# Kernel optimization log

Measured on AMD Instinct MI355X. Metric: run time of the kernel, lower is better.

The kernel has to match this reference:

```python
import jax, jax.numpy as jnp
import numpy as np

LOCAL_FEATURE_WEIGHT = 1.0  # hypers['local_feature_weight']
HIDDEN = 256
X_DIM = 64
N_NODES = 512
N_GLOBAL = 8
MLP_HID = [512, 256]
N_OUT = 2


def _glorot(key, shape):
    lim = np.sqrt(6.0 / (shape[0] + shape[1]))
    return jax.random.uniform(key, shape, jnp.float32, -lim, lim)


def setup_inputs() -> dict:
    key = jax.random.key(0)
    ks = jax.random.split(key, 16)
    inp = {
        'seq': jax.random.normal(ks[0], (1024, N_NODES, X_DIM), jnp.float32),
        'global_features': jax.random.normal(ks[1], (1024, N_GLOBAL), jnp.float32),
    }
    # GRU cell params (TF GRUCell layout): gate kernel [x+h, 2h], candidate kernel [x+h, h]
    D = X_DIM + HIDDEN
    inp['fw_gw'] = _glorot(ks[2], (D, 2 * HIDDEN))
    inp['fw_gb'] = jnp.ones((2 * HIDDEN,), jnp.float32)  # TF GRUCell gate bias init = 1.0
    inp['fw_cw'] = _glorot(ks[3], (D, HIDDEN))
    inp['fw_cb'] = jnp.zeros((HIDDEN,), jnp.float32)
    inp['bw_gw'] = _glorot(ks[4], (D, 2 * HIDDEN))
    inp['bw_gb'] = jnp.ones((2 * HIDDEN,), jnp.float32)
    inp['bw_cw'] = _glorot(ks[5], (D, HIDDEN))
    inp['bw_cb'] = jnp.zeros((HIDDEN,), jnp.float32)
    # output MLP: in = 4*HIDDEN + N_GLOBAL -> 512 -> 256 -> 2
    d_in = 4 * HIDDEN + N_GLOBAL
    inp['w1'] = _glorot(ks[6], (d_in, MLP_HID[0]))
    inp['b1'] = jnp.zeros((MLP_HID[0],), jnp.float32)
    inp['w2'] = _glorot(ks[7], (MLP_HID[0], MLP_HID[1]))
    inp['b2'] = jnp.zeros((MLP_HID[1],), jnp.float32)
    inp['w3'] = _glorot(ks[8], (MLP_HID[1], N_OUT))
    inp['b3'] = jnp.zeros((N_OUT,), jnp.float32)
    return inp


def _gru_final(gw, gb, cw, cb, x):
    """TF GRUCell over x [B,T,D]; returns final hidden state [B,H]."""
    H = cb.shape[0]
    B = x.shape[0]

    def step(h, xt):
        xh = jnp.concatenate([xt, h], axis=1)
        ru = jax.nn.sigmoid(xh @ gw + gb)
        r, u = ru[:, :H], ru[:, H:]
        c = jnp.tanh(jnp.concatenate([xt, r * h], axis=1) @ cw + cb)
        h_new = u * h + (1.0 - u) * c
        return h_new, None

    h0 = jnp.zeros((B, H), x.dtype)
    hT, _ = jax.lax.scan(step, h0, jnp.swapaxes(x, 0, 1))
    return hT


def reference(seq, global_features, fw_gw, fw_gb, fw_cw, fw_cb,
              bw_gw, bw_gb, bw_cw, bw_cb, w1, b1, w2, b2, w3, b3):
    half = seq.shape[1] // 2
    target = seq[:, :half, :]
    probe = seq[:, half:, :]

    # bidirectional_dynamic_rnn final states: fw over seq, bw over reversed seq
    tgt_fw = _gru_final(fw_gw, fw_gb, fw_cw, fw_cb, target)
    tgt_bw = _gru_final(bw_gw, bw_gb, bw_cw, bw_cb, target[:, ::-1, :])
    prb_fw = _gru_final(fw_gw, fw_gb, fw_cw, fw_cb, probe)
    prb_bw = _gru_final(bw_gw, bw_gb, bw_cw, bw_cb, probe[:, ::-1, :])

    h = jnp.concatenate([tgt_fw, tgt_bw, prb_fw, prb_bw], axis=1)  # [B, 4H]
    h = jnp.concatenate([LOCAL_FEATURE_WEIGHT * h, global_features], axis=1)

    h = jax.nn.relu(h @ w1 + b1)
    h = jax.nn.relu(h @ w2 + b2)
    out = h @ w3 + b3  # [B, 2]

    pred_mean = out[:, 0]
    pred_precision = jnp.abs(out[:, 1])
    return jnp.stack([pred_mean, pred_precision], axis=1)  # [B, 2]
```

## Files before the change

kernel.cpp:

```cpp
#include <hip/hip_runtime.h>
#include <hip/hip_bf16.h>
#include <hip/hip_fp16.h>

typedef __attribute__((ext_vector_type(8))) short bf16x8;
typedef __attribute__((ext_vector_type(4))) short bf16x4;
typedef __attribute__((ext_vector_type(4))) float f32x4;
typedef __attribute__((ext_vector_type(4))) int   i32x4;

static __device__ __forceinline__ unsigned short f2bf(float f) {
  unsigned u = __float_as_uint(f);
  u += 0x7fffu + ((u >> 16) & 1u);
  return (unsigned short)(u >> 16);
}
static __device__ __forceinline__ short fb(float f) {
  union { __hip_bfloat16 b; short s; } u;
  u.b = __float2bfloat16(f);
  return u.s;
}
static __device__ __forceinline__ float sigm(float x) {
  return __builtin_amdgcn_rcpf(1.0f + __expf(-x));
}
static __device__ __forceinline__ float tanh_fast(float x) {
  return 2.0f * __builtin_amdgcn_rcpf(1.0f + __expf(-2.0f * x)) - 1.0f;
}
static __device__ __forceinline__ bf16x8 pack8(float4 a, float4 b) {
  bf16x8 v;
  v[0] = fb(a.x); v[1] = fb(a.y); v[2] = fb(a.z); v[3] = fb(a.w);
  v[4] = fb(b.x); v[5] = fb(b.y); v[6] = fb(b.z); v[7] = fb(b.w);
  return v;
}
static __device__ __forceinline__ void pin8(bf16x8& v) {
  i32x4 t;
  __builtin_memcpy(&t, &v, 16);
  asm volatile("" : "+v"(t));
  __builtin_memcpy(&v, &t, 16);
}

static __device__ __forceinline__ void lds_barrier() {
  __builtin_amdgcn_sched_barrier(0);
  asm volatile("s_waitcnt lgkmcnt(0)" ::: "memory");
  __builtin_amdgcn_s_barrier();
  __builtin_amdgcn_sched_barrier(0);
}

__global__ void prep_weights(const float* __restrict__ fw_gw, const float* __restrict__ fw_cw,
                             const float* __restrict__ bw_gw, const float* __restrict__ bw_cw,
                             unsigned short* __restrict__ wT) {
  int gid = blockIdx.x * 256 + threadIdx.x;
  int kg = gid % 80;
  int n  = (gid / 80) % 768;
  int s  = gid / (80 * 768);
  if (s >= 2) return;
  const float* gw = s ? bw_gw : fw_gw;
  const float* cw = s ? bw_cw : fw_cw;
  unsigned short* dst = wT + ((size_t)s * 768 + n) * 320 + kg * 4;
  #pragma unroll
  for (int j = 0; j < 4; ++j) {
    int k = kg * 4 + j;
    float v = (n < 512) ? gw[(size_t)k * 512 + n] : cw[(size_t)k * 256 + (n - 512)];
    dst[j] = f2bf(v);
  }
}

__global__ __attribute__((amdgpu_flat_work_group_size(512, 512), amdgpu_waves_per_eu(2, 2)))
void gru_kernel(
    const float* __restrict__ seq,
    const float* __restrict__ fw_gb, const float* __restrict__ fw_cb,
    const float* __restrict__ bw_gb, const float* __restrict__ bw_cb,
    const unsigned short* __restrict__ wT,
    float* __restrict__ h_cat) {
  __shared__ unsigned short wcLDS[256 * 256];
  __shared__ char shAB[16384];
  __shared__ __align__(16) float gbL[768];

  const int tid  = threadIdx.x;
  const int w    = tid >> 6;
  const int lane = tid & 63;
  const int l15  = lane & 15;
  const int lk   = lane >> 4;
  const int ci   = blockIdx.x >> 6;
  const int rb   = blockIdx.x & 63;
  const int s    = ci & 1;
  const int tbase = (ci >> 1) * 256;

  const unsigned short* wg = wT + (size_t)s * (768 * 320);
  const unsigned short* wc = wg + (size_t)512 * 320;
  const float* gbp = s ? bw_gb : fw_gb;
  const float* cbp = s ? bw_cb : fw_cb;

  for (int i = tid; i < 8192; i += 512) {
    const int l15s = i & 15, lks = (i >> 4) & 3, kks = (i >> 6) & 7, c16 = i >> 9;
    bf16x8 v = *(const bf16x8*)(wc + (size_t)(c16 * 16 + l15s) * 320 + 64 + kks * 32 + lks * 8);
    *(bf16x8*)((char*)wcLDS + (size_t)i * 16) = v;
  }
  for (int i = tid; i < 2048; i += 512) ((int*)shAB)[i] = 0;
  for (int i = tid; i < 768; i += 512) gbL[i] = (i < 512) ? gbp[i] : cbp[i - 512];

  const int colr = w * 32;

  bf16x8 wgr[4][10];
  #pragma unroll
  for (int nt = 0; nt < 4; ++nt) {
    const int col = (nt < 2) ? (colr + nt * 16) : (256 + colr + (nt - 2) * 16);
    const unsigned short* base = wg + (size_t)(col + l15) * 320;
    #pragma unroll
    for (int kk = 0; kk < 10; ++kk) {
      const int k = (kk < 8) ? (64 + kk * 32) : ((kk - 8) * 32);
      wgr[nt][kk] = *(const bf16x8*)(base + k + lk * 8);
    }
  }
  bf16x8 wcx[2][2];
  #pragma unroll
  for (int nt = 0; nt < 2; ++nt) {
    const unsigned short* base = wc + (size_t)(colr + nt * 16 + l15) * 320;
    #pragma unroll
    for (int kt = 0; kt < 2; ++kt)
      wcx[nt][kt] = *(const bf16x8*)(base + kt * 32 + lk * 8);
  }
  #pragma unroll
  for (int nt = 0; nt < 4; ++nt)
    #pragma unroll
    for (int kk = 0; kk < 10; ++kk) pin8(wgr[nt][kk]);
  #pragma unroll
  for (int nt = 0; nt < 2; ++nt) { pin8(wcx[nt][0]); pin8(wcx[nt][1]); }

  const int rdA = lk * 256 + l15 * 16;
  int rdB[2], wrB[2];
  #pragma unroll
  for (int nt = 0; nt < 2; ++nt) {
    rdB[nt] = (w * 2 + nt) * 8192 + lk * 256 + l15 * 16;
    const int c0 = colr + nt * 16 + lk * 4;
    wrB[nt] = ((c0 >> 5) << 10) + (((c0 >> 3) & 3) << 8) + l15 * 16 + ((c0 & 7) << 1);
  }

  const float* pseq = seq + (size_t)(rb * 16 + l15) * 32768 + lk * 8
                    + (size_t)(tbase + (s ? 255 : 0)) * 64;
  const int dstep = s ? -64 : 64;

  f32x4 hreg[2];
  hreg[0] = (f32x4)(0.f); hreg[1] = (f32x4)(0.f);

  float4 q0 = *(const float4*)(pseq);
  float4 q1 = *(const float4*)(pseq + 4);
  float4 q2 = *(const float4*)(pseq + 32);
  float4 q3 = *(const float4*)(pseq + 36);

  __syncthreads();

  #pragma unroll 1
  for (int t = 0; t < 256; ++t) {
    bf16x8 xf0 = pack8(q0, q1);
    bf16x8 xf1 = pack8(q2, q3);
    if (t != 255) {
      pseq += dstep;
      q0 = *(const float4*)(pseq);
      q1 = *(const float4*)(pseq + 4);
      q2 = *(const float4*)(pseq + 32);
      q3 = *(const float4*)(pseq + 36);
    }

    f32x4 acc1[4];
    #pragma unroll
    for (int nt = 0; nt < 4; ++nt) {
      const int g0 = ((nt < 2) ? (colr + nt * 16) : (256 + colr + (nt - 2) * 16)) + lk * 4;
      acc1[nt] = *(const f32x4*)&gbL[g0];
    }
    #pragma unroll
    for (int kk = 0; kk < 8; ++kk) {
      bf16x8 hf = *(const bf16x8*)(shAB + rdA + kk * 1024);
      #pragma unroll
      for (int nt = 0; nt < 4; ++nt)
        acc1[nt] = __builtin_amdgcn_mfma_f32_16x16x32_bf16(wgr[nt][kk], hf, acc1[nt], 0, 0, 0);
    }
    #pragma unroll
    for (int nt = 0; nt < 4; ++nt)
      acc1[nt] = __builtin_amdgcn_mfma_f32_16x16x32_bf16(wgr[nt][8], xf0, acc1[nt], 0, 0, 0);
    #pragma unroll
    for (int nt = 0; nt < 4; ++nt)
      acc1[nt] = __builtin_amdgcn_mfma_f32_16x16x32_bf16(wgr[nt][9], xf1, acc1[nt], 0, 0, 0);

    #pragma unroll
    for (int nt = 0; nt < 2; ++nt) {
      bf16x4 rhw;
      #pragma unroll
      for (int i = 0; i < 4; ++i)
        rhw[i] = fb(sigm(acc1[nt][i]) * hreg[nt][i]);
      *(bf16x4*)(shAB + 8192 + wrB[nt]) = rhw;
    }
    lds_barrier();

    f32x4 acc2[2];
    #pragma unroll
    for (int nt = 0; nt < 2; ++nt)
      acc2[nt] = *(const f32x4*)&gbL[512 + colr + nt * 16 + lk * 4];
    #pragma unroll
    for (int kk = 0; kk < 8; ++kk) {
      bf16x8 rh = *(const bf16x8*)(shAB + 8192 + rdA + kk * 1024);
      #pragma unroll
      for (int nt = 0; nt < 2; ++nt) {
        bf16x8 b = *(const bf16x8*)((const char*)wcLDS + rdB[nt] + kk * 1024);
        acc2[nt] = __builtin_amdgcn_mfma_f32_16x16x32_bf16(b, rh, acc2[nt], 0, 0, 0);
      }
    }
    #pragma unroll
    for (int nt = 0; nt < 2; ++nt) {
      acc2[nt] = __builtin_amdgcn_mfma_f32_16x16x32_bf16(wcx[nt][0], xf0, acc2[nt], 0, 0, 0);
      acc2[nt] = __builtin_amdgcn_mfma_f32_16x16x32_bf16(wcx[nt][1], xf1, acc2[nt], 0, 0, 0);
    }

    const bool last = (t == 255);
    #pragma unroll
    for (int nt = 0; nt < 2; ++nt) {
      bf16x4 hw;
      float hc[4];
      #pragma unroll
      for (int i = 0; i < 4; ++i) {
        const float cv = tanh_fast(acc2[nt][i]);
        const float u  = sigm(acc1[nt + 2][i]);
        const float hn = u * hreg[nt][i] + (1.f - u) * cv;
        hreg[nt][i] = hn;
        hw[i] = fb(hn);
        hc[i] = hn;
      }
      *(bf16x4*)(shAB + wrB[nt]) = hw;
      if (last) {
        float4 o; o.x = hc[0]; o.y = hc[1]; o.z = hc[2]; o.w = hc[3];
        *(float4*)&h_cat[(size_t)(rb * 16 + l15) * 1024 + ci * 256 + colr + nt * 16 + lk * 4] = o;
      }
    }
    lds_barrier();
  }
}

__global__ __launch_bounds__(256) void mlp1(const float* __restrict__ h_cat,
                                            const float* __restrict__ gf,
                                            const float* __restrict__ w1,
                                            const float* __restrict__ b1,
                                            float* __restrict__ a1) {
  __shared__ float xs[8][1036];
  const int tid = threadIdx.x;
  const int r0 = blockIdx.x * 8;
  for (int i = tid; i < 8 * 1032; i += 256) {
    int m = i / 1032, k = i - m * 1032;
    xs[m][k] = (k < 1024) ? h_cat[(size_t)(r0 + m) * 1024 + k]
                          : gf[(size_t)(r0 + m) * 8 + (k - 1024)];
  }
  __syncthreads();
  float acc0[8], acc1v[8];
  #pragma unroll
  for (int m = 0; m < 8; ++m) { acc0[m] = 0.f; acc1v[m] = 0.f; }
  const int n = tid;
  for (int k = 0; k < 1032; k += 4) {
    float wa[4], wb[4];
    #pragma unroll
    for (int j = 0; j < 4; ++j) {
      wa[j] = w1[(size_t)(k + j) * 512 + n];
      wb[j] = w1[(size_t)(k + j) * 512 + n + 256];
    }
    #pragma unroll
    for (int m = 0; m < 8; ++m) {
      float4 xv = *(const float4*)&xs[m][k];
      acc0[m]  = fmaf(xv.w, wa[3], fmaf(xv.z, wa[2], fmaf(xv.y, wa[1], fmaf(xv.x, wa[0], acc0[m]))));
      acc1v[m] = fmaf(xv.w, wb[3], fmaf(xv.z, wb[2], fmaf(xv.y, wb[1], fmaf(xv.x, wb[0], acc1v[m]))));
    }
  }
  const float bb0 = b1[n], bb1 = b1[n + 256];
  #pragma unroll
  for (int m = 0; m < 8; ++m) {
    a1[(size_t)(r0 + m) * 512 + n]       = fmaxf(acc0[m] + bb0, 0.f);
    a1[(size_t)(r0 + m) * 512 + n + 256] = fmaxf(acc1v[m] + bb1, 0.f);
  }
}

__global__ __launch_bounds__(256) void mlp2(const float* __restrict__ a1,
                                            const float* __restrict__ w2,
                                            const float* __restrict__ b2,
                                            float* __restrict__ a2) {
  __shared__ float xs[8][516];
  const int tid = threadIdx.x;
  const int r0 = blockIdx.x * 8;
  for (int i = tid; i < 8 * 512; i += 256) {
    int m = i >> 9, k = i & 511;
    xs[m][k] = a1[(size_t)(r0 + m) * 512 + k];
  }
  __syncthreads();
  float acc[8];
  #pragma unroll
  for (int m = 0; m < 8; ++m) acc[m] = 0.f;
  for (int k = 0; k < 512; k += 4) {
    float wa[4];
    #pragma unroll
    for (int j = 0; j < 4; ++j) wa[j] = w2[(size_t)(k + j) * 256 + tid];
    #pragma unroll
    for (int m = 0; m < 8; ++m) {
      float4 xv = *(const float4*)&xs[m][k];
      acc[m] = fmaf(xv.w, wa[3], fmaf(xv.z, wa[2], fmaf(xv.y, wa[1], fmaf(xv.x, wa[0], acc[m]))));
    }
  }
  const float bb = b2[tid];
  #pragma unroll
  for (int m = 0; m < 8; ++m)
    a2[(size_t)(r0 + m) * 256 + tid] = fmaxf(acc[m] + bb, 0.f);
}

__global__ __launch_bounds__(256) void mlp3(const float* __restrict__ a2,
                                            const float* __restrict__ w3,
                                            const float* __restrict__ b3,
                                            float* __restrict__ out) {
  const int r = blockIdx.x * 256 + threadIdx.x;
  float m = 0.f, p = 0.f;
  for (int k = 0; k < 256; k += 4) {
    float4 v = *(const float4*)&a2[(size_t)r * 256 + k];
    m = fmaf(v.x, w3[2 * k],     fmaf(v.y, w3[2 * k + 2], fmaf(v.z, w3[2 * k + 4], fmaf(v.w, w3[2 * k + 6], m))));
    p = fmaf(v.x, w3[2 * k + 1], fmaf(v.y, w3[2 * k + 3], fmaf(v.z, w3[2 * k + 5], fmaf(v.w, w3[2 * k + 7], p))));
  }
  out[2 * r]     = m + b3[0];
  out[2 * r + 1] = fabsf(p + b3[1]);
}

extern "C" void kernel_launch(void* const* d_in, const int* in_sizes, int n_in,
                              void* d_out, int out_size, void* d_ws, size_t ws_size,
                              hipStream_t stream) {
  const float* seq   = (const float*)d_in[0];
  const float* gf    = (const float*)d_in[1];
  const float* fw_gw = (const float*)d_in[2];
  const float* fw_gb = (const float*)d_in[3];
  const float* fw_cw = (const float*)d_in[4];
  const float* fw_cb = (const float*)d_in[5];
  const float* bw_gw = (const float*)d_in[6];
  const float* bw_gb = (const float*)d_in[7];
  const float* bw_cw = (const float*)d_in[8];
  const float* bw_cb = (const float*)d_in[9];
  const float* w1 = (const float*)d_in[10];
  const float* b1 = (const float*)d_in[11];
  const float* w2 = (const float*)d_in[12];
  const float* b2 = (const float*)d_in[13];
  const float* w3 = (const float*)d_in[14];
  const float* b3 = (const float*)d_in[15];
  float* out = (float*)d_out;

  char* ws = (char*)d_ws;
  unsigned short* wT = (unsigned short*)(ws);
  float* h_cat = (float*)(ws + 983040);
  float* a1    = (float*)(ws + 983040 + 4194304);
  float* a2    = (float*)(ws + 983040 + 4194304 + 2097152);

  hipLaunchKernelGGL(prep_weights, dim3(480), dim3(256), 0, stream,
                     fw_gw, fw_cw, bw_gw, bw_cw, wT);
  hipLaunchKernelGGL(gru_kernel, dim3(256), dim3(512), 0, stream,
                     seq, fw_gb, fw_cb, bw_gb, bw_cb, wT, h_cat);
  hipLaunchKernelGGL(mlp1, dim3(128), dim3(256), 0, stream, h_cat, gf, w1, b1, a1);
  hipLaunchKernelGGL(mlp2, dim3(128), dim3(256), 0, stream, a1, w2, b2, a2);
  hipLaunchKernelGGL(mlp3, dim3(4), dim3(256), 0, stream, a2, w3, b3, out);
}
```

Measured before the change: 723.9 us.

## Move x-input MFMAs off the recurrent critical path and split accumulator chains

The input-projection MFMAs for the next timestep's gate accumulators are issued at the end of the current step, after the hidden-state write. The candidate's x-projection is issued before the LDS barrier rather than after the r*h matmul. The r*h matmul uses two interleaved accumulators to shorten the dependent MFMA chain, and the update-gate sigmoid is computed early. The aim is to cut serial latency per recurrent step. The cost is extra registers and a slightly different summation order.

```diff
diff --git a/kernel.cpp b/kernel.cpp
--- a/kernel.cpp
+++ b/kernel.cpp
@@ -144,90 +144,108 @@
   float4 q1 = *(const float4*)(pseq + 4);
   float4 q2 = *(const float4*)(pseq + 32);
   float4 q3 = *(const float4*)(pseq + 36);
+  bf16x8 xf0 = pack8(q0, q1);
+  bf16x8 xf1 = pack8(q2, q3);
+  pseq += dstep;
+  q0 = *(const float4*)(pseq);
+  q1 = *(const float4*)(pseq + 4);
+  q2 = *(const float4*)(pseq + 32);
+  q3 = *(const float4*)(pseq + 36);
 
   __syncthreads();
+
+  f32x4 acc1[4];
+  #pragma unroll
+  for (int nt = 0; nt < 4; ++nt) {
+    const int g0 = ((nt < 2) ? (colr + nt * 16) : (256 + colr + (nt - 2) * 16)) + lk * 4;
+    acc1[nt] = *(const f32x4*)&gbL[g0];
+    acc1[nt] = __builtin_amdgcn_mfma_f32_16x16x32_bf16(wgr[nt][8], xf0, acc1[nt], 0, 0, 0);
+    acc1[nt] = __builtin_amdgcn_mfma_f32_16x16x32_bf16(wgr[nt][9], xf1, acc1[nt], 0, 0, 0);
+  }
 
   #pragma unroll 1
   for (int t = 0; t < 256; ++t) {
-    bf16x8 xf0 = pack8(q0, q1);
-    bf16x8 xf1 = pack8(q2, q3);
-    if (t != 255) {
-      pseq += dstep;
+    #pragma unroll
+    for (int kk = 0; kk < 8; ++kk) {
+      bf16x8 hf = *(const bf16x8*)(shAB + rdA + kk * 1024);
+      #pragma unroll
+      for (int nt = 0; nt < 4; ++nt)
+        acc1[nt] = __builtin_amdgcn_mfma_f32_16x16x32_bf16(wgr[nt][kk], hf, acc1[nt], 0, 0, 0);
+    }
+
+    float ur[2][4];
+    #pragma unroll
+    for (int nt = 0; nt < 2; ++nt) {
+      bf16x4 rhw;
+      #pragma unroll
+      for (int i = 0; i < 4; ++i) {
+        rhw[i] = fb(sigm(acc1[nt][i]) * hreg[nt][i]);
+        ur[nt][i] = sigm(acc1[nt + 2][i]);
+      }
+      *(bf16x4*)(shAB + 8192 + wrB[nt]) = rhw;
+    }
+
+    f32x4 acc2[2];
+    #pragma unroll
+    for (int nt = 0; nt < 2; ++nt) {
+      acc2[nt] = *(const f32x4*)&gbL[512 + colr + nt * 16 + lk * 4];
+      acc2[nt] = __builtin_amdgcn_mfma_f32_16x16x32_bf16(wcx[nt][0], xf0, acc2[nt], 0, 0, 0);
+      acc2[nt] = __builtin_amdgcn_mfma_f32_16x16x32_bf16(wcx[nt][1], xf1, acc2[nt], 0, 0, 0);
+    }
+
+    lds_barrier();
+
+    f32x4 acc2o[2];
+    acc2o[0] = (f32x4)(0.f); acc2o[1] = (f32x4)(0.f);
+    #pragma unroll
+    for (int kk = 0; kk < 8; ++kk) {
+      bf16x8 rh = *(const bf16x8*)(shAB + 8192 + rdA + kk * 1024);
+      #pragma unroll
+      for (int nt = 0; nt < 2; ++nt) {
+        bf16x8 b = *(const bf16x8*)((const char*)wcLDS + rdB[nt] + kk * 1024);
+        if (kk & 1)
+          acc2o[nt] = __builtin_amdgcn_mfma_f32_16x16x32_bf16(b, rh, acc2o[nt], 0, 0, 0);
+        else
+          acc2[nt]  = __builtin_amdgcn_mfma_f32_16x16x32_bf16(b, rh, acc2[nt], 0, 0, 0);
+      }
+    }
+
+    const bool last = (t == 255);
+    #pragma unroll
+    for (int nt = 0; nt < 2; ++nt) {
+      f32x4 a2 = acc2[nt] + acc2o[nt];
+      bf16x4 hw;
+      #pragma unroll
+      for (int i = 0; i < 4; ++i) {
+        const float cv = tanh_fast(a2[i]);
+        const float hn = cv + ur[nt][i] * (hreg[nt][i] - cv);
+        hreg[nt][i] = hn;
+        hw[i] = fb(hn);
+      }
+      *(bf16x4*)(shAB + wrB[nt]) = hw;
+      if (last) {
+        float4 o; o.x = hreg[nt][0]; o.y = hreg[nt][1]; o.z = hreg[nt][2]; o.w = hreg[nt][3];
+        *(float4*)&h_cat[(size_t)(rb * 16 + l15) * 1024 + ci * 256 + colr + nt * 16 + lk * 4] = o;
+      }
+    }
+
+    if (t < 255) {
+      xf0 = pack8(q0, q1);
+      xf1 = pack8(q2, q3);
+      pseq = (t < 254) ? (pseq + dstep) : pseq;
       q0 = *(const float4*)(pseq);
       q1 = *(const float4*)(pseq + 4);
       q2 = *(const float4*)(pseq + 32);
       q3 = *(const float4*)(pseq + 36);
-    }
-
-    f32x4 acc1[4];
-    #pragma unroll
-    for (int nt = 0; nt < 4; ++nt) {
-      const int g0 = ((nt < 2) ? (colr + nt * 16) : (256 + colr + (nt - 2) * 16)) + lk * 4;
-      acc1[nt] = *(const f32x4*)&gbL[g0];
-    }
-    #pragma unroll
-    for (int kk = 0; kk < 8; ++kk) {
-      bf16x8 hf = *(const bf16x8*)(shAB + rdA + kk * 1024);
-      #pragma unroll
-      for (int nt = 0; nt < 4; ++nt)
-        acc1[nt] = __builtin_amdgcn_mfma_f32_16x16x32_bf16(wgr[nt][kk], hf, acc1[nt], 0, 0, 0);
-    }
-    #pragma unroll
-    for (int nt = 0; nt < 4; ++nt)
-      acc1[nt] = __builtin_amdgcn_mfma_f32_16x16x32_bf16(wgr[nt][8], xf0, acc1[nt], 0, 0, 0);
-    #pragma unroll
-    for (int nt = 0; nt < 4; ++nt)
-      acc1[nt] = __builtin_amdgcn_mfma_f32_16x16x32_bf16(wgr[nt][9], xf1, acc1[nt], 0, 0, 0);
-
-    #pragma unroll
-    for (int nt = 0; nt < 2; ++nt) {
-      bf16x4 rhw;
-      #pragma unroll
-      for (int i = 0; i < 4; ++i)
-        rhw[i] = fb(sigm(acc1[nt][i]) * hreg[nt][i]);
-      *(bf16x4*)(shAB + 8192 + wrB[nt]) = rhw;
-    }
-    lds_barrier();
-
-    f32x4 acc2[2];
-    #pragma unroll
-    for (int nt = 0; nt < 2; ++nt)
-      acc2[nt] = *(const f32x4*)&gbL[512 + colr + nt * 16 + lk * 4];
-    #pragma unroll
-    for (int kk = 0; kk < 8; ++kk) {
-      bf16x8 rh = *(const bf16x8*)(shAB + 8192 + rdA + kk * 1024);
-      #pragma unroll
-      for (int nt = 0; nt < 2; ++nt) {
-        bf16x8 b = *(const bf16x8*)((const char*)wcLDS + rdB[nt] + kk * 1024);
-        acc2[nt] = __builtin_amdgcn_mfma_f32_16x16x32_bf16(b, rh, acc2[nt], 0, 0, 0);
-      }
-    }
-    #pragma unroll
-    for (int nt = 0; nt < 2; ++nt) {
-      acc2[nt] = __builtin_amdgcn_mfma_f32_16x16x32_bf16(wcx[nt][0], xf0, acc2[nt], 0, 0, 0);
-      acc2[nt] = __builtin_amdgcn_mfma_f32_16x16x32_bf16(wcx[nt][1], xf1, acc2[nt], 0, 0, 0);
-    }
-
-    const bool last = (t == 255);
-    #pragma unroll
-    for (int nt = 0; nt < 2; ++nt) {
-      bf16x4 hw;
-      float hc[4];
-      #pragma unroll
-      for (int i = 0; i < 4; ++i) {
-        const float cv = tanh_fast(acc2[nt][i]);
-        const float u  = sigm(acc1[nt + 2][i]);
-        const float hn = u * hreg[nt][i] + (1.f - u) * cv;
-        hreg[nt][i] = hn;
-        hw[i] = fb(hn);
-        hc[i] = hn;
-      }
-      *(bf16x4*)(shAB + wrB[nt]) = hw;
-      if (last) {
-        float4 o; o.x = hc[0]; o.y = hc[1]; o.z = hc[2]; o.w = hc[3];
-        *(float4*)&h_cat[(size_t)(rb * 16 + l15) * 1024 + ci * 256 + colr + nt * 16 + lk * 4] = o;
-      }
-    }
+      #pragma unroll
+      for (int nt = 0; nt < 4; ++nt) {
+        const int g0 = ((nt < 2) ? (colr + nt * 16) : (256 + colr + (nt - 2) * 16)) + lk * 4;
+        acc1[nt] = *(const f32x4*)&gbL[g0];
+        acc1[nt] = __builtin_amdgcn_mfma_f32_16x16x32_bf16(wgr[nt][8], xf0, acc1[nt], 0, 0, 0);
+        acc1[nt] = __builtin_amdgcn_mfma_f32_16x16x32_bf16(wgr[nt][9], xf1, acc1[nt], 0, 0, 0);
+      }
+    }
+
     lds_barrier();
   }
 }
```

Result: slower. 954.7 us (+31.9%).
